# Kernel optimization log

Measured on AMD Instinct MI355X. Metric: run time of the kernel, lower is better.

Reference implementation:

```python
import jax, jax.numpy as jnp
import numpy as np

H = 24; W = 24; N = H * W            # board tokens
R = 4; BINS = (2 * R + 1) ** 2 + 1    # 82 rel-pos bins (far bin = 81)
G = 2                                  # num_global_tokens
T = N + 1 + G                          # cls + globals + board tokens = 579
D = 256; NH = 8; HD = D // NH
DEPTH = 6; MLP = int(D * 2.0)
B = 16; CIN = 10


def _ln(x, g, b):
    m = jnp.mean(x, axis=-1, keepdims=True)
    v = jnp.mean(jnp.square(x - m), axis=-1, keepdims=True)
    return (x - m) * jax.lax.rsqrt(v + 1e-5) * g + b


def _head(x, g, b, w1, b1, w2, b2):
    h = _ln(x, g, b)
    h = jax.nn.gelu(h @ w1 + b1, approximate=False)
    return h @ w2 + b2


def _forward(obs, input_w, input_b, cls_token, global_tokens, row_embed, col_embed,
             ln1_g, ln1_b, qkv_w, qkv_b, proj_w, proj_b, rel_bias,
             ln2_g, ln2_b, fc1_w, fc1_b, fc2_w, fc2_b,
             norm_g, norm_b,
             pol_ln_g, pol_ln_b, pol_w1, pol_b1, pol_w2, pol_b2,
             val_ln_g, val_ln_b, val_w1, val_b1, val_w2, val_b2,
             rel_idx):
    Bsz = obs.shape[0]
    # _tokens_from_obs: (B, C, H, W) -> (B, N, C); channel order is already [revealed, counts]
    tokens = obs.reshape(Bsz, CIN, N).transpose(0, 2, 1)
    x = tokens @ input_w + input_b                                    # (B, N, D)
    pos = (row_embed[:, None, :] + col_embed[None, :, :]).reshape(N, D)
    x = x + pos
    x = jnp.concatenate([jnp.broadcast_to(cls_token, (Bsz, 1, D)),
                         jnp.broadcast_to(global_tokens, (Bsz, G, D)),
                         x], axis=1)                                   # (B, T, D)
    scale = 1.0 / jnp.sqrt(jnp.float32(HD))

    def block(x, p):
        l1g, l1b, qw, qb, pw, pb, rb, l2g, l2b, f1w, f1b, f2w, f2b = p
        h = _ln(x, l1g, l1b)
        qkv = (h @ qw + qb).reshape(Bsz, T, 3, NH, HD)
        q, k, v = qkv[:, :, 0], qkv[:, :, 1], qkv[:, :, 2]             # (B, T, NH, HD)
        bias = rb[:, rel_idx]                                          # (NH, T, T) gathered bias
        scores = jnp.einsum('bqhd,bkhd->bhqk', q, k) * scale + bias[None]
        probs = jax.nn.softmax(scores, axis=-1)
        o = jnp.einsum('bhqk,bkhd->bqhd', probs, v).reshape(Bsz, T, D)
        x = x + o @ pw + pb
        h2 = _ln(x, l2g, l2b)
        x = x + jax.nn.gelu(h2 @ f1w + f1b, approximate=False) @ f2w + f2b
        return x, None

    params = (ln1_g, ln1_b, qkv_w, qkv_b, proj_w, proj_b, rel_bias,
              ln2_g, ln2_b, fc1_w, fc1_b, fc2_w, fc2_b)
    x, _ = jax.lax.scan(block, x, params)
    x = _ln(x, norm_g, norm_b)
    cls_tok = x[:, 0]
    token_states = x[:, 1:N + 1]   # faithful to source slice (includes the global tokens)
    logits = _head(token_states, pol_ln_g, pol_ln_b, pol_w1, pol_b1, pol_w2, pol_b2)[..., 0]  # (B, N)
    value = _head(cls_tok, val_ln_g, val_ln_b, val_w1, val_b1, val_w2, val_b2)                 # (B, 1)
    return jnp.concatenate([logits, value], axis=1)  # (B, N+1)


def setup_inputs() -> dict:
    keys = iter(jax.random.split(jax.random.key(0), 40))
    def p(shape, s=0.02):
        return jax.random.normal(next(keys), shape, jnp.float32) * s
    # _build_rel_pos_index, embedded into full (T, T) buffer with far_bin elsewhere
    coords = np.stack(np.meshgrid(np.arange(H), np.arange(W), indexing='ij'), -1).reshape(-1, 2)
    rel = coords[:, None, :] - coords[None, :, :]
    far = (np.abs(rel) > R).any(-1)
    rel = np.clip(rel, -R, R) + R
    idx = rel[..., 0] * (2 * R + 1) + rel[..., 1]
    idx = np.where(far, BINS - 1, idx)
    full = np.full((T, T), BINS - 1, np.int32)
    full[1:N + 1, 1:N + 1] = idx
    return {
        'obs': jax.random.normal(next(keys), (B, CIN, H, W), jnp.float32),
        'input_w': p((CIN, D)), 'input_b': jnp.zeros((D,)),
        'cls_token': jnp.zeros((1, 1, D)),
        'global_tokens': jnp.zeros((1, G, D)),
        'row_embed': p((H, D)), 'col_embed': p((W, D)),
        'ln1_g': jnp.ones((DEPTH, D)), 'ln1_b': jnp.zeros((DEPTH, D)),
        'qkv_w': p((DEPTH, D, 3 * D)), 'qkv_b': jnp.zeros((DEPTH, 3 * D)),
        'proj_w': p((DEPTH, D, D)), 'proj_b': jnp.zeros((DEPTH, D)),
        'rel_bias': p((DEPTH, NH, BINS)),
        'ln2_g': jnp.ones((DEPTH, D)), 'ln2_b': jnp.zeros((DEPTH, D)),
        'fc1_w': p((DEPTH, D, MLP)), 'fc1_b': jnp.zeros((DEPTH, MLP)),
        'fc2_w': p((DEPTH, MLP, D)), 'fc2_b': jnp.zeros((DEPTH, D)),
        'norm_g': jnp.ones((D,)), 'norm_b': jnp.zeros((D,)),
        'pol_ln_g': jnp.ones((D,)), 'pol_ln_b': jnp.zeros((D,)),
        'pol_w1': p((D, D)), 'pol_b1': jnp.zeros((D,)),
        'pol_w2': p((D, 1)), 'pol_b2': jnp.zeros((1,)),
        'val_ln_g': jnp.ones((D,)), 'val_ln_b': jnp.zeros((D,)),
        'val_w1': p((D, D)), 'val_b1': jnp.zeros((D,)),
        'val_w2': p((D, 1)), 'val_b2': jnp.zeros((1,)),
        'rel_idx': jnp.asarray(full),
    }


def reference(obs, input_w, input_b, cls_token, global_tokens, row_embed, col_embed,
              ln1_g, ln1_b, qkv_w, qkv_b, proj_w, proj_b, rel_bias,
              ln2_g, ln2_b, fc1_w, fc1_b, fc2_w, fc2_b,
              norm_g, norm_b,
              pol_ln_g, pol_ln_b, pol_w1, pol_b1, pol_w2, pol_b2,
              val_ln_g, val_ln_b, val_w1, val_b1, val_w2, val_b2,
              rel_idx):
    return _forward(obs, input_w, input_b, cls_token, global_tokens, row_embed, col_embed,
                    ln1_g, ln1_b, qkv_w, qkv_b, proj_w, proj_b, rel_bias,
                    ln2_g, ln2_b, fc1_w, fc1_b, fc2_w, fc2_b,
                    norm_g, norm_b,
                    pol_ln_g, pol_ln_b, pol_w1, pol_b1, pol_w2, pol_b2,
                    val_ln_g, val_ln_b, val_w1, val_b1, val_w2, val_b2,
                    rel_idx)
```

## Files before the change

### kernel.cpp

```cpp
#include <hip/hip_runtime.h>
#include <math.h>

constexpr int Hc = 24, Wc = 24, Nc = 576, BINSc = 82, Gc = 2;
constexpr int Tc = Nc + 1 + Gc;
constexpr int Dc = 256, NHc = 8, HDc = 32, DEPTHc = 6, MLPc = 512;
constexpr int Bc = 16, CINc = 10;
constexpr int BT = Bc * Tc;
constexpr float SCALE = 0.17677669529663687f;

typedef _Float16 f16;
typedef _Float16 f16x8 __attribute__((ext_vector_type(8)));
typedef _Float16 f16x16 __attribute__((ext_vector_type(16)));
typedef float f32x4 __attribute__((ext_vector_type(4)));

constexpr size_t QK_ST   = (size_t)BT * 256;
constexpr int    VT_PAD  = 640;
constexpr size_t VT_ST   = (size_t)Bc * NHc * 32 * VT_PAD;
constexpr size_t OFF_KH  = 2 * QK_ST;
constexpr size_t OFF_VTH = 4 * QK_ST;
constexpr size_t OFF_BIAS = 4 * QK_ST + 2 * VT_ST;
constexpr int    BPAD    = 580;
constexpr size_t R_F16   = OFF_BIAS + (size_t)NHc * Tc * BPAD;
constexpr size_t R_FLOATS = 8707904;

__device__ __forceinline__ int xcd_swz(int d, int nwg) {
    const int q = nwg >> 3, r = nwg & 7;
    const int x = d & 7, s = d >> 3;
    return x * q + (x < r ? x : r) + s;
}

__device__ __forceinline__ float gelu_f(float x) {
    return 0.5f * x * (1.0f + erff(x * 0.70710678118654752f));
}

__device__ __forceinline__ float block_sum256(float v, float* s4) {
    #pragma unroll
    for (int off = 32; off > 0; off >>= 1) v += __shfl_down(v, off, 64);
    __syncthreads();
    if ((threadIdx.x & 63) == 0) s4[threadIdx.x >> 6] = v;
    __syncthreads();
    return s4[0] + s4[1] + s4[2] + s4[3];
}

__global__ __launch_bounds__(256) void embed_kernel(
        const float* __restrict__ obs, const float* __restrict__ iw,
        const float* __restrict__ ib, const float* __restrict__ cls,
        const float* __restrict__ glob, const float* __restrict__ rowe,
        const float* __restrict__ cole, float* __restrict__ x) {
    int t = blockIdx.x, b = blockIdx.y, d = threadIdx.x;
    float v;
    if (t == 0) {
        v = cls[d];
    } else if (t <= Gc) {
        v = glob[(t - 1) * Dc + d];
    } else {
        int n = t - 1 - Gc;
        float acc = ib[d];
        #pragma unroll
        for (int c = 0; c < CINc; ++c)
            acc = fmaf(obs[(b * CINc + c) * Nc + n], iw[c * Dc + d], acc);
        v = acc + rowe[(n / Wc) * Dc + d] + cole[(n % Wc) * Dc + d];
    }
    x[((size_t)b * Tc + t) * Dc + d] = v;
}

__global__ __launch_bounds__(256) void ln4_kernel(
        const float* __restrict__ x, const float* __restrict__ g,
        const float* __restrict__ b, float* __restrict__ out, int nrows) {
    const int w = threadIdx.x >> 6, l = threadIdx.x & 63;
    const int row = blockIdx.x * 4 + w;
    if (row >= nrows) return;
    const float4 v = *reinterpret_cast<const float4*>(x + (size_t)row * Dc + l * 4);
    float s = v.x + v.y + v.z + v.w;
    #pragma unroll
    for (int mk = 1; mk < 64; mk <<= 1) s += __shfl_xor(s, mk, 64);
    const float m = s * (1.0f / 256.0f);
    const float4 d = make_float4(v.x - m, v.y - m, v.z - m, v.w - m);
    float vs = d.x * d.x + d.y * d.y + d.z * d.z + d.w * d.w;
    #pragma unroll
    for (int mk = 1; mk < 64; mk <<= 1) vs += __shfl_xor(vs, mk, 64);
    const float rs = rsqrtf(vs * (1.0f / 256.0f) + 1e-5f);
    const float4 gg = *reinterpret_cast<const float4*>(g + l * 4);
    const float4 bb = *reinterpret_cast<const float4*>(b + l * 4);
    *reinterpret_cast<float4*>(out + (size_t)row * Dc + l * 4) =
        make_float4(d.x * rs * gg.x + bb.x, d.y * rs * gg.y + bb.y,
                    d.z * rs * gg.z + bb.z, d.w * rs * gg.w + bb.w);
}

__global__ __launch_bounds__(256) void lnsel4_kernel(
        const float* __restrict__ xn, const float* __restrict__ g,
        const float* __restrict__ b, float* __restrict__ out) {
    const int w = threadIdx.x >> 6, l = threadIdx.x & 63;
    const int rr = blockIdx.x * 4 + w;
    const int bb = rr / Nc, n = rr % Nc;
    const float* xr = xn + ((size_t)bb * Tc + 1 + n) * Dc;
    const float4 v = *reinterpret_cast<const float4*>(xr + l * 4);
    float s = v.x + v.y + v.z + v.w;
    #pragma unroll
    for (int mk = 1; mk < 64; mk <<= 1) s += __shfl_xor(s, mk, 64);
    const float m = s * (1.0f / 256.0f);
    const float4 d = make_float4(v.x - m, v.y - m, v.z - m, v.w - m);
    float vs = d.x * d.x + d.y * d.y + d.z * d.z + d.w * d.w;
    #pragma unroll
    for (int mk = 1; mk < 64; mk <<= 1) vs += __shfl_xor(vs, mk, 64);
    const float rs = rsqrtf(vs * (1.0f / 256.0f) + 1e-5f);
    const float4 gg = *reinterpret_cast<const float4*>(g + l * 4);
    const float4 bb4 = *reinterpret_cast<const float4*>(b + l * 4);
    *reinterpret_cast<float4*>(out + ((size_t)bb * Nc + n) * Dc + l * 4) =
        make_float4(d.x * rs * gg.x + bb4.x, d.y * rs * gg.y + bb4.y,
                    d.z * rs * gg.z + bb4.z, d.w * rs * gg.w + bb4.w);
}

__global__ __launch_bounds__(256) void split_w_kernel(
        const float* __restrict__ qkv_w, const float* __restrict__ proj_w,
        const float* __restrict__ fc1_w, const float* __restrict__ fc2_w,
        const float* __restrict__ pol_w1, f16* __restrict__ out) {
    int r = blockIdx.x * 256 + threadIdx.x;
    float v; f16* dst; int NK;
    if (r < 1179648) {
        int layer = r / 196608, e = r % 196608;
        int n = e >> 8, k = e & 255;
        v = qkv_w[(size_t)layer * 196608 + k * 768 + n];
        dst = out + (size_t)layer * 393216 + n * 256 + k; NK = 196608;
    } else if (r < 1572864) {
        int rr = r - 1179648; int layer = rr / 65536, e = rr % 65536;
        int n = e >> 8, k = e & 255;
        v = proj_w[(size_t)layer * 65536 + k * 256 + n];
        dst = out + 2359296 + (size_t)layer * 131072 + n * 256 + k; NK = 65536;
    } else if (r < 2359296) {
        int rr = r - 1572864; int layer = rr / 131072, e = rr % 131072;
        int n = e >> 8, k = e & 255;
        v = fc1_w[(size_t)layer * 131072 + k * 512 + n];
        dst = out + 3145728 + (size_t)layer * 262144 + n * 256 + k; NK = 131072;
    } else if (r < 3145728) {
        int rr = r - 2359296; int layer = rr / 131072, e = rr % 131072;
        int n = e >> 9, k = e & 511;
        v = fc2_w[(size_t)layer * 131072 + k * 256 + n];
        dst = out + 4718592 + (size_t)layer * 262144 + n * 512 + k; NK = 131072;
    } else if (r < 3211264) {
        int rr = r - 3145728; int n = rr >> 8, k = rr & 255;
        v = pol_w1[k * 256 + n];
        dst = out + 6291456 + n * 256 + k; NK = 65536;
    } else return;
    f16 h = (f16)v;
    dst[0] = h;
    dst[NK] = (f16)(v - (float)h);
}

__global__ __launch_bounds__(256) void biasgen_kernel(
        const float* __restrict__ relb, const int* __restrict__ relidx,
        f16* __restrict__ bias) {
    const int q = blockIdx.x, h = blockIdx.y;
    const size_t rowo = ((size_t)h * Tc + q) * BPAD;
    const int* ridx = relidx + q * Tc;
    const float* rb = relb + h * BINSc;
    for (int kp = threadIdx.x; kp * 2 + 1 < Tc; kp += 256) {
        f16 b0 = (f16)rb[ridx[kp * 2]];
        f16 b1 = (f16)rb[ridx[kp * 2 + 1]];
        unsigned pk = (unsigned)__builtin_bit_cast(unsigned short, b0) |
                      ((unsigned)__builtin_bit_cast(unsigned short, b1) << 16);
        *reinterpret_cast<unsigned*>(&bias[rowo + kp * 2]) = pk;
    }
    if (threadIdx.x == 0)
        bias[rowo + Tc - 1] = (f16)rb[ridx[Tc - 1]];
}

__device__ __forceinline__ int swz(int r, int g) {
    return r * 40 + ((g ^ ((r >> 3) & 3)) << 3);
}
template <int ACT, bool RES>
__global__ __launch_bounds__(256) void mgemm_kernel(
        const float* __restrict__ A, const f16* __restrict__ WT,
        const float* __restrict__ bias, const float* __restrict__ res,
        float* __restrict__ C, int M, int N, int K, int nbx) {
    constexpr int BM = 128, BN = 64, BK = 32;
    __shared__ f16 Ah[BM * 40], Al[BM * 40];
    __shared__ f16 Bh[BN * 40], Bl[BN * 40];
    const int tid = threadIdx.x;
    const int v = xcd_swz(blockIdx.x, gridDim.x);
    const int m0 = (v / nbx) * BM, n0 = (v % nbx) * BN;
    const int w = tid >> 6, l = tid & 63;
    const int wm = (w >> 1) * 64, wn = (w & 1) * 32;
    const int lg = l >> 4, lr = l & 15;
    f32x4 acc[4][2] = {};
    const int sa_row = tid >> 1, sa_kc = (tid & 1) * 16;
    const int sb_part = tid >> 7;
    const int sb_n = (tid & 127) >> 1, sb_kc = (tid & 1) * 16;

    for (int k0 = 0; k0 < K; k0 += BK) {
        {
            int gr = m0 + sa_row; if (gr >= M) gr = M - 1;
            const float4* src = reinterpret_cast<const float4*>(
                A + (size_t)gr * K + k0 + sa_kc);
            f16x8 hv0, hv1, lv0, lv1;
            #pragma unroll
            for (int c = 0; c < 4; ++c) {
                float4 v4 = src[c];
                f16 h0 = (f16)v4.x, h1 = (f16)v4.y, h2 = (f16)v4.z, h3 = (f16)v4.w;
                f16 l0 = (f16)(v4.x - (float)h0), l1 = (f16)(v4.y - (float)h1);
                f16 l2 = (f16)(v4.z - (float)h2), l3 = (f16)(v4.w - (float)h3);
                if (c < 2) {
                    hv0[c * 4 + 0] = h0; hv0[c * 4 + 1] = h1;
                    hv0[c * 4 + 2] = h2; hv0[c * 4 + 3] = h3;
                    lv0[c * 4 + 0] = l0; lv0[c * 4 + 1] = l1;
                    lv0[c * 4 + 2] = l2; lv0[c * 4 + 3] = l3;
                } else {
                    hv1[(c - 2) * 4 + 0] = h0; hv1[(c - 2) * 4 + 1] = h1;
                    hv1[(c - 2) * 4 + 2] = h2; hv1[(c - 2) * 4 + 3] = h3;
                    lv1[(c - 2) * 4 + 0] = l0; lv1[(c - 2) * 4 + 1] = l1;
                    lv1[(c - 2) * 4 + 2] = l2; lv1[(c - 2) * 4 + 3] = l3;
                }
            }
            const int g0 = sa_kc >> 3;
            *reinterpret_cast<f16x8*>(&Ah[swz(sa_row, g0)])     = hv0;
            *reinterpret_cast<f16x8*>(&Ah[swz(sa_row, g0 + 1)]) = hv1;
            *reinterpret_cast<f16x8*>(&Al[swz(sa_row, g0)])     = lv0;
            *reinterpret_cast<f16x8*>(&Al[swz(sa_row, g0 + 1)]) = lv1;
        }
        {
            const f16x8* src = reinterpret_cast<const f16x8*>(
                WT + (size_t)sb_part * N * K + (size_t)(n0 + sb_n) * K + k0 + sb_kc);
            f16* dbase = sb_part ? Bl : Bh;
            const int g0 = sb_kc >> 3;
            *reinterpret_cast<f16x8*>(&dbase[swz(sb_n, g0)])     = src[0];
            *reinterpret_cast<f16x8*>(&dbase[swz(sb_n, g0 + 1)]) = src[1];
        }
        __syncthreads();
        f16x8 afh[4], afl[4], bfh[2], bfl[2];
        #pragma unroll
        for (int mi = 0; mi < 4; ++mi) {
            int row = wm + mi * 16 + lr;
            afh[mi] = *reinterpret_cast<const f16x8*>(&Ah[swz(row, lg)]);
            afl[mi] = *reinterpret_cast<const f16x8*>(&Al[swz(row, lg)]);
        }
        #pragma unroll
        for (int ni = 0; ni < 2; ++ni) {
            int col = wn + ni * 16 + lr;
            bfh[ni] = *reinterpret_cast<const f16x8*>(&Bh[swz(col, lg)]);
            bfl[ni] = *reinterpret_cast<const f16x8*>(&Bl[swz(col, lg)]);
        }
        #pragma unroll
        for (int mi = 0; mi < 4; ++mi)
            #pragma unroll
            for (int ni = 0; ni < 2; ++ni) {
                acc[mi][ni] = __builtin_amdgcn_mfma_f32_16x16x32_f16(
                    afh[mi], bfh[ni], acc[mi][ni], 0, 0, 0);
                acc[mi][ni] = __builtin_amdgcn_mfma_f32_16x16x32_f16(
                    afh[mi], bfl[ni], acc[mi][ni], 0, 0, 0);
                acc[mi][ni] = __builtin_amdgcn_mfma_f32_16x16x32_f16(
                    afl[mi], bfh[ni], acc[mi][ni], 0, 0, 0);
            }
        __syncthreads();
    }
    float bv[2];
    #pragma unroll
    for (int ni = 0; ni < 2; ++ni) bv[ni] = bias[n0 + wn + ni * 16 + lr];
    #pragma unroll
    for (int mi = 0; mi < 4; ++mi) {
        #pragma unroll
        for (int r = 0; r < 4; ++r) {
            int grow = m0 + wm + mi * 16 + lg * 4 + r;
            if (grow >= M) continue;
            if constexpr (ACT == 2) {
                f16* base = (f16*)C;
                const int bb = grow / Tc;
                const int tt = grow - bb * Tc;
                #pragma unroll
                for (int ni = 0; ni < 2; ++ni) {
                    const int gcol = n0 + wn + ni * 16 + lr;
                    float vv = acc[mi][ni][r] + bv[ni];
                    if (gcol < 256) {
                        vv *= SCALE;
                        f16 hh = (f16)vv;
                        base[(size_t)grow * 256 + gcol] = hh;
                        base[QK_ST + (size_t)grow * 256 + gcol] = (f16)(vv - (float)hh);
                    } else if (gcol < 512) {
                        f16 hh = (f16)vv;
                        base[OFF_KH + (size_t)grow * 256 + (gcol - 256)] = hh;
                        base[OFF_KH + QK_ST + (size_t)grow * 256 + (gcol - 256)] =
                            (f16)(vv - (float)hh);
                    } else {
                        const int e = gcol - 512;
                        const int hh_ = e >> 5, dd = e & 31;
                        const size_t o =
                            ((size_t)((bb * NHc + hh_) * 32 + dd)) * VT_PAD + tt;
                        f16 hh = (f16)vv;
                        base[OFF_VTH + o] = hh;
                        base[OFF_VTH + VT_ST + o] = (f16)(vv - (float)hh);
                    }
                }
            } else {
                #pragma unroll
                for (int ni = 0; ni < 2; ++ni) {
                    int gcol = n0 + wn + ni * 16 + lr;
                    float vv = acc[mi][ni][r] + bv[ni];
                    if (ACT == 1) vv = gelu_f(vv);
                    if (RES) vv += res[(size_t)grow * N + gcol];
                    C[(size_t)grow * N + gcol] = vv;
                }
            }
        }
    }
}

__global__ __launch_bounds__(256, 4) void mattn2_kernel(
        const f16* __restrict__ qsp, float* __restrict__ o) {
    __shared__ __align__(16) f16 Kh_s[64][40], Kl_s[64][40];
    __shared__ __align__(16) f16 VTh_s[32][72], VTl_s[32][72];
    __shared__ __align__(16) f16 Ph_s[4][16][72], Pl_s[4][16][72];
    const f16* __restrict__ Kh_g  = qsp + OFF_KH;
    const f16* __restrict__ VTh_g = qsp + OFF_VTH;
    const f16* __restrict__ bias_g = qsp + OFF_BIAS;

    const int tid = threadIdx.x;
    const int v = xcd_swz(blockIdx.x, 1280);
    const int bh = v / 10, qt = v - bh * 10;
    const int b = bh >> 3, h = bh & 7;
    const int q0 = qt * 64;
    const int w = tid >> 6, l = tid & 63;
    const int lr = l & 15, lg = l >> 4;

    int qrow = q0 + w * 16 + lr; if (qrow >= Tc) qrow = Tc - 1;
    const f16* qp = qsp + ((size_t)(b * Tc + qrow)) * 256 + h * 32 + lg * 8;
    const f16x8 Qh = *reinterpret_cast<const f16x8*>(qp);
    const f16x8 Ql = *reinterpret_cast<const f16x8*>(qp + QK_ST);
    const int myq = q0 + w * 16 + lg * 4;

    int boff[4];
    #pragma unroll
    for (int r = 0; r < 4; ++r) {
        int qq = myq + r; if (qq >= Tc) qq = Tc - 1;
        boff[r] = (h * Tc + qq) * BPAD;
    }

    const int skrow = tid >> 2, skc = (tid & 3) * 8;
    const int svd = tid >> 3, svc = (tid & 7) * 8;
    const f16* vrow = VTh_g + ((size_t)((b * NHc + h) * 32 + svd)) * VT_PAD;

    struct KV { f16x8 kh, kl, vh, vl; };
    auto load_kv = [&](int k0) {
        KV r;
        int gk = k0 + skrow; if (gk >= Tc) gk = Tc - 1;
        const f16* kp = Kh_g + ((size_t)(b * Tc + gk)) * 256 + h * 32 + skc;
        r.kh = *reinterpret_cast<const f16x8*>(kp);
        r.kl = *reinterpret_cast<const f16x8*>(kp + QK_ST);
        const f16* vp = vrow + k0 + svc;
        r.vh = *reinterpret_cast<const f16x8*>(vp);
        r.vl = *reinterpret_cast<const f16x8*>(vp + VT_ST);
        return r;
    };
    auto load_bias = [&](int k0) {
        f16x16 bv;
        #pragma unroll
        for (int r = 0; r < 4; ++r)
            #pragma unroll
            for (int j = 0; j < 4; ++j) {
                int kk = k0 + j * 16 + lr; if (kk >= Tc) kk = Tc - 1;
                bv[r * 4 + j] = bias_g[boff[r] + kk];
            }
        return bv;
    };

    KV pA = load_kv(0);
    KV pB = load_kv(64);
    f16x16 bias_c = load_bias(0), bias_n;

    float m_run[4], l_run[4];
    f32x4 Oacc[2] = {};
    #pragma unroll
    for (int r = 0; r < 4; ++r) { m_run[r] = -1e30f; l_run[r] = 0.f; }

    for (int t = 0; t < 10; ++t) {
        const int k0 = t * 64;
        __syncthreads();
        *reinterpret_cast<f16x8*>(&Kh_s[skrow][skc]) = pA.kh;
        *reinterpret_cast<f16x8*>(&Kl_s[skrow][skc]) = pA.kl;
        *reinterpret_cast<f16x8*>(&VTh_s[svd][svc]) = pA.vh;
        *reinterpret_cast<f16x8*>(&VTl_s[svd][svc]) = pA.vl;
        pA = pB;
        if (t + 2 < 10) pB = load_kv(k0 + 128);
        __syncthreads();
        if (t + 1 < 10) bias_n = load_bias(k0 + 64);
        f32x4 sc[4];
        #pragma unroll
        for (int j = 0; j < 4; ++j) {
            const f16x8 kh = *reinterpret_cast<const f16x8*>(&Kh_s[j * 16 + lr][lg * 8]);
            const f16x8 kl = *reinterpret_cast<const f16x8*>(&Kl_s[j * 16 + lr][lg * 8]);
            f32x4 s = {};
            s = __builtin_amdgcn_mfma_f32_16x16x32_f16(Qh, kh, s, 0, 0, 0);
            s = __builtin_amdgcn_mfma_f32_16x16x32_f16(Qh, kl, s, 0, 0, 0);
            s = __builtin_amdgcn_mfma_f32_16x16x32_f16(Ql, kh, s, 0, 0, 0);
            sc[j] = s;
        }
        #pragma unroll
        for (int r = 0; r < 4; ++r)
            #pragma unroll
            for (int j = 0; j < 4; ++j) {
                const int kk = k0 + j * 16 + lr;
                float vv = sc[j][r] + (float)bias_c[r * 4 + j];
                sc[j][r] = (kk < Tc) ? vv : -1e30f;
            }
        #pragma unroll
        for (int r = 0; r < 4; ++r) {
            float tm = fmaxf(fmaxf(sc[0][r], sc[1][r]), fmaxf(sc[2][r], sc[3][r]));
            #pragma unroll
            for (int mk = 1; mk < 16; mk <<= 1) tm = fmaxf(tm, __shfl_xor(tm, mk, 64));
            const float mn = fmaxf(m_run[r], tm);
            const float resc = __expf(m_run[r] - mn);
            m_run[r] = mn;
            float ls = 0.f;
            #pragma unroll
            for (int j = 0; j < 4; ++j) {
                sc[j][r] = __expf(sc[j][r] - mn);
                ls += sc[j][r];
            }
            #pragma unroll
            for (int mk = 1; mk < 16; mk <<= 1) ls += __shfl_xor(ls, mk, 64);
            l_run[r] = l_run[r] * resc + ls;
            Oacc[0][r] *= resc; Oacc[1][r] *= resc;
            const int prow = lg * 4 + r;
            #pragma unroll
            for (int j = 0; j < 4; ++j) {
                const float p = sc[j][r];
                const f16 ph = (f16)p;
                Ph_s[w][prow][j * 16 + lr] = ph;
                Pl_s[w][prow][j * 16 + lr] = (f16)(p - (float)ph);
            }
        }
        #pragma unroll
        for (int kc = 0; kc < 2; ++kc) {
            const f16x8 Pa = *reinterpret_cast<const f16x8*>(&Ph_s[w][lr][kc * 32 + lg * 8]);
            const f16x8 Pb = *reinterpret_cast<const f16x8*>(&Pl_s[w][lr][kc * 32 + lg * 8]);
            #pragma unroll
            for (int dt = 0; dt < 2; ++dt) {
                const f16x8 vh = *reinterpret_cast<const f16x8*>(&VTh_s[dt * 16 + lr][kc * 32 + lg * 8]);
                const f16x8 vl = *reinterpret_cast<const f16x8*>(&VTl_s[dt * 16 + lr][kc * 32 + lg * 8]);
                Oacc[dt] = __builtin_amdgcn_mfma_f32_16x16x32_f16(Pa, vh, Oacc[dt], 0, 0, 0);
                Oacc[dt] = __builtin_amdgcn_mfma_f32_16x16x32_f16(Pa, vl, Oacc[dt], 0, 0, 0);
                Oacc[dt] = __builtin_amdgcn_mfma_f32_16x16x32_f16(Pb, vh, Oacc[dt], 0, 0, 0);
            }
        }
        if (t + 1 < 10) bias_c = bias_n;
    }
    #pragma unroll
    for (int r = 0; r < 4; ++r) {
        const int qq = myq + r;
        if (qq < Tc) {
            const float inv = 1.0f / l_run[r];
            float* op = o + ((size_t)b * Tc + qq) * Dc + h * HDc;
            op[lr]      = Oacc[0][r] * inv;
            op[16 + lr] = Oacc[1][r] * inv;
        }
    }
}

__global__ __launch_bounds__(256) void logits_kernel(
        const float* __restrict__ ph, const float* __restrict__ w2,
        const float* __restrict__ b2, float* __restrict__ out) {
    __shared__ float s4[4];
    size_t r = blockIdx.x;
    int bb = (int)(r / Nc), n = (int)(r % Nc);
    float v = ph[r * Dc + threadIdx.x] * w2[threadIdx.x];
    float s = block_sum256(v, s4);
    if (threadIdx.x == 0) out[bb * (Nc + 1) + n] = s + b2[0];
}

__global__ __launch_bounds__(256) void value_kernel(
        const float* __restrict__ xn, const float* __restrict__ g,
        const float* __restrict__ b, const float* __restrict__ w1,
        const float* __restrict__ b1, const float* __restrict__ w2,
        const float* __restrict__ b2, float* __restrict__ out) {
    __shared__ float s4[4];
    __shared__ float ts[Dc];
    const int bb = blockIdx.x, tid = threadIdx.x;
    float v = xn[(size_t)bb * Tc * Dc + tid];
    float m = block_sum256(v, s4) * (1.0f / 256.0f);
    float d = v - m;
    float var = block_sum256(d * d, s4) * (1.0f / 256.0f);
    ts[tid] = d * rsqrtf(var + 1e-5f) * g[tid] + b[tid];
    __syncthreads();
    float acc = b1[tid];
    #pragma unroll 8
    for (int i = 0; i < Dc; ++i) acc = fmaf(ts[i], w1[i * Dc + tid], acc);
    float hv = gelu_f(acc) * w2[tid];
    float s = block_sum256(hv, s4);
    if (tid == 0) out[bb * (Nc + 1) + Nc] = s + b2[0];
}

extern "C" void kernel_launch(void* const* d_in, const int* in_sizes, int n_in,
                              void* d_out, int out_size, void* d_ws, size_t ws_size,
                              hipStream_t stream) {
    const float* obs      = (const float*)d_in[0];
    const float* input_w  = (const float*)d_in[1];
    const float* input_b  = (const float*)d_in[2];
    const float* cls_tok  = (const float*)d_in[3];
    const float* glob_tok = (const float*)d_in[4];
    const float* row_emb  = (const float*)d_in[5];
    const float* col_emb  = (const float*)d_in[6];
    const float* ln1_g    = (const float*)d_in[7];
    const float* ln1_b    = (const float*)d_in[8];
    const float* qkv_w    = (const float*)d_in[9];
    const float* qkv_b    = (const float*)d_in[10];
    const float* proj_w   = (const float*)d_in[11];
    const float* proj_b   = (const float*)d_in[12];
    const float* rel_bias = (const float*)d_in[13];
    const float* ln2_g    = (const float*)d_in[14];
    const float* ln2_b    = (const float*)d_in[15];
    const float* fc1_w    = (const float*)d_in[16];
    const float* fc1_b    = (const float*)d_in[17];
    const float* fc2_w    = (const float*)d_in[18];
    const float* fc2_b    = (const float*)d_in[19];
    const float* norm_g   = (const float*)d_in[20];
    const float* norm_b   = (const float*)d_in[21];
    const float* pol_ln_g = (const float*)d_in[22];
    const float* pol_ln_b = (const float*)d_in[23];
    const float* pol_w1   = (const float*)d_in[24];
    const float* pol_b1   = (const float*)d_in[25];
    const float* pol_w2   = (const float*)d_in[26];
    const float* pol_b2   = (const float*)d_in[27];
    const float* val_ln_g = (const float*)d_in[28];
    const float* val_ln_b = (const float*)d_in[29];
    const float* val_w1   = (const float*)d_in[30];
    const float* val_b1   = (const float*)d_in[31];
    const float* val_w2   = (const float*)d_in[32];
    const float* val_b2   = (const float*)d_in[33];
    const int*   rel_idx  = (const int*)d_in[34];
    float* out = (float*)d_out;

    float* ws = (float*)d_ws;
    const size_t SZ_XD = (size_t)BT * Dc;
    float* X  = ws;
    float* Hb = ws + SZ_XD;
    float* R  = ws + 2 * SZ_XD;
    f16* qsp = (f16*)R;
    f16* bias_g = qsp + OFF_BIAS;
    float* MLPH = R;
    float* PT = R;
    float* PH = R + (size_t)Bc * Nc * Dc;
    f16* wsplit = (f16*)(R + R_FLOATS);

    auto qkvT = [&](int l) { return wsplit + (size_t)l * 393216; };
    auto projT = [&](int l) { return wsplit + 2359296 + (size_t)l * 131072; };
    auto fc1T = [&](int l) { return wsplit + 3145728 + (size_t)l * 262144; };
    auto fc2T = [&](int l) { return wsplit + 4718592 + (size_t)l * 262144; };
    f16* polT = wsplit + 6291456;

    split_w_kernel<<<12544, 256, 0, stream>>>(
        qkv_w, proj_w, fc1_w, fc2_w, pol_w1, wsplit);

    embed_kernel<<<dim3(Tc, Bc), 256, 0, stream>>>(
        obs, input_w, input_b, cls_tok, glob_tok, row_emb, col_emb, X);

    for (int l = 0; l < DEPTHc; ++l) {
        ln4_kernel<<<(BT + 3) / 4, 256, 0, stream>>>(
            X, ln1_g + l * Dc, ln1_b + l * Dc, Hb, BT);
        mgemm_kernel<2, false><<<876, 256, 0, stream>>>(
            Hb, qkvT(l), qkv_b + l * 3 * Dc, nullptr, (float*)qsp, BT, 3 * Dc, Dc, 12);
        biasgen_kernel<<<dim3(Tc, NHc), 256, 0, stream>>>(
            rel_bias + l * NHc * BINSc, rel_idx, bias_g);
        mattn2_kernel<<<1280, 256, 0, stream>>>(qsp, Hb);
        mgemm_kernel<0, true><<<292, 256, 0, stream>>>(
            Hb, projT(l), proj_b + l * Dc, X, X, BT, Dc, Dc, 4);
        ln4_kernel<<<(BT + 3) / 4, 256, 0, stream>>>(
            X, ln2_g + l * Dc, ln2_b + l * Dc, Hb, BT);
        mgemm_kernel<1, false><<<584, 256, 0, stream>>>(
            Hb, fc1T(l), fc1_b + l * MLPc, nullptr, MLPH, BT, MLPc, Dc, 8);
        mgemm_kernel<0, true><<<292, 256, 0, stream>>>(
            MLPH, fc2T(l), fc2_b + l * Dc, X, X, BT, Dc, MLPc, 4);
    }

    ln4_kernel<<<(BT + 3) / 4, 256, 0, stream>>>(X, norm_g, norm_b, Hb, BT);
    lnsel4_kernel<<<Bc * Nc / 4, 256, 0, stream>>>(Hb, pol_ln_g, pol_ln_b, PT);
    mgemm_kernel<1, false><<<288, 256, 0, stream>>>(
        PT, polT, pol_b1, nullptr, PH, Bc * Nc, Dc, Dc, 4);
    logits_kernel<<<Bc * Nc, 256, 0, stream>>>(PH, pol_w2, pol_b2, out);
    value_kernel<<<Bc, 256, 0, stream>>>(
        Hb, val_ln_g, val_ln_b, val_w1, val_b1, val_w2, val_b2, out);
}
```

Measured before the change: 1.314 ms.

## Fuse LayerNorm apply into GEMM A-load and compute softmax denominator via MFMA

```diff
diff --git a/kernel.cpp b/kernel.cpp
--- a/kernel.cpp
+++ b/kernel.cpp
@@ -62,6 +62,24 @@
         v = acc + rowe[(n / Wc) * Dc + d] + cole[(n % Wc) * Dc + d];
     }
     x[((size_t)b * Tc + t) * Dc + d] = v;
+}
+
+__global__ __launch_bounds__(256) void lnstats_kernel(
+        const float* __restrict__ x, float2* __restrict__ st, int nrows) {
+    const int w = threadIdx.x >> 6, l = threadIdx.x & 63;
+    const int row = blockIdx.x * 4 + w;
+    if (row >= nrows) return;
+    const float4 v = *reinterpret_cast<const float4*>(x + (size_t)row * Dc + l * 4);
+    float s = v.x + v.y + v.z + v.w;
+    #pragma unroll
+    for (int mk = 1; mk < 64; mk <<= 1) s += __shfl_xor(s, mk, 64);
+    const float m = s * (1.0f / 256.0f);
+    float vs = (v.x - m) * (v.x - m) + (v.y - m) * (v.y - m) +
+               (v.z - m) * (v.z - m) + (v.w - m) * (v.w - m);
+    #pragma unroll
+    for (int mk = 1; mk < 64; mk <<= 1) vs += __shfl_xor(vs, mk, 64);
+    if (l == 0)
+        st[row] = make_float2(m, rsqrtf(vs * (1.0f / 256.0f) + 1e-5f));
 }
 
 __global__ __launch_bounds__(256) void ln4_kernel(
@@ -168,11 +186,13 @@
 __device__ __forceinline__ int swz(int r, int g) {
     return r * 40 + ((g ^ ((r >> 3) & 3)) << 3);
 }
-template <int ACT, bool RES>
+template <int ACT, bool RES, bool LNA>
 __global__ __launch_bounds__(256) void mgemm_kernel(
         const float* __restrict__ A, const f16* __restrict__ WT,
         const float* __restrict__ bias, const float* __restrict__ res,
-        float* __restrict__ C, int M, int N, int K, int nbx) {
+        float* __restrict__ C, int M, int N, int K, int nbx,
+        const float2* __restrict__ lnst, const float* __restrict__ lng,
+        const float* __restrict__ lnb) {
     constexpr int BM = 128, BN = 64, BK = 32;
     __shared__ f16 Ah[BM * 40], Al[BM * 40];
     __shared__ f16 Bh[BN * 40], Bl[BN * 40];
@@ -187,15 +207,28 @@
     const int sb_part = tid >> 7;
     const int sb_n = (tid & 127) >> 1, sb_kc = (tid & 1) * 16;
 
+    int gr = m0 + sa_row; if (gr >= M) gr = M - 1;
+    float mu = 0.f, rsd = 1.f;
+    if constexpr (LNA) { float2 s2 = lnst[gr]; mu = s2.x; rsd = s2.y; }
+
     for (int k0 = 0; k0 < K; k0 += BK) {
         {
-            int gr = m0 + sa_row; if (gr >= M) gr = M - 1;
             const float4* src = reinterpret_cast<const float4*>(
                 A + (size_t)gr * K + k0 + sa_kc);
             f16x8 hv0, hv1, lv0, lv1;
             #pragma unroll
             for (int c = 0; c < 4; ++c) {
                 float4 v4 = src[c];
+                if constexpr (LNA) {
+                    const float4 g4 = *reinterpret_cast<const float4*>(
+                        lng + k0 + sa_kc + c * 4);
+                    const float4 b4 = *reinterpret_cast<const float4*>(
+                        lnb + k0 + sa_kc + c * 4);
+                    v4.x = (v4.x - mu) * rsd * g4.x + b4.x;
+                    v4.y = (v4.y - mu) * rsd * g4.y + b4.y;
+                    v4.z = (v4.z - mu) * rsd * g4.z + b4.z;
+                    v4.w = (v4.w - mu) * rsd * g4.w + b4.w;
+                }
                 f16 h0 = (f16)v4.x, h1 = (f16)v4.y, h2 = (f16)v4.z, h3 = (f16)v4.w;
                 f16 l0 = (f16)(v4.x - (float)h0), l1 = (f16)(v4.y - (float)h1);
                 f16 l2 = (f16)(v4.z - (float)h2), l3 = (f16)(v4.w - (float)h3);
@@ -314,8 +347,9 @@
 
     const int tid = threadIdx.x;
     const int v = xcd_swz(blockIdx.x, 1280);
-    const int bh = v / 10, qt = v - bh * 10;
-    const int b = bh >> 3, h = bh & 7;
+    const int h = v / 160;
+    const int rem = v - h * 160;
+    const int b = rem / 10, qt = rem - b * 10;
     const int q0 = qt * 64;
     const int w = tid >> 6, l = tid & 63;
     const int lr = l & 15, lg = l >> 4;
@@ -365,10 +399,15 @@
     KV pB = load_kv(64);
     f16x16 bias_c = load_bias(0), bias_n;
 
-    float m_run[4], l_run[4];
+    f16x8 kOnes;
+    #pragma unroll
+    for (int e = 0; e < 8; ++e) kOnes[e] = (f16)1.0f;
+
+    float m_run[4];
     f32x4 Oacc[2] = {};
-    #pragma unroll
-    for (int r = 0; r < 4; ++r) { m_run[r] = -1e30f; l_run[r] = 0.f; }
+    f32x4 Oext = {};
+    #pragma unroll
+    for (int r = 0; r < 4; ++r) m_run[r] = -1e30f;
 
     for (int t = 0; t < 10; ++t) {
         const int k0 = t * 64;
@@ -386,20 +425,18 @@
         for (int j = 0; j < 4; ++j) {
             const f16x8 kh = *reinterpret_cast<const f16x8*>(&Kh_s[j * 16 + lr][lg * 8]);
             const f16x8 kl = *reinterpret_cast<const f16x8*>(&Kl_s[j * 16 + lr][lg * 8]);
-            f32x4 s = {};
+            f32x4 s = {(float)bias_c[j], (float)bias_c[4 + j],
+                       (float)bias_c[8 + j], (float)bias_c[12 + j]};
             s = __builtin_amdgcn_mfma_f32_16x16x32_f16(Qh, kh, s, 0, 0, 0);
             s = __builtin_amdgcn_mfma_f32_16x16x32_f16(Qh, kl, s, 0, 0, 0);
             s = __builtin_amdgcn_mfma_f32_16x16x32_f16(Ql, kh, s, 0, 0, 0);
             sc[j] = s;
         }
         #pragma unroll
-        for (int r = 0; r < 4; ++r)
-            #pragma unroll
-            for (int j = 0; j < 4; ++j) {
-                const int kk = k0 + j * 16 + lr;
-                float vv = sc[j][r] + (float)bias_c[r * 4 + j];
-                sc[j][r] = (kk < Tc) ? vv : -1e30f;
-            }
+        for (int j = 0; j < 4; ++j) {
+            const int kk = k0 + j * 16 + lr;
+            if (kk >= Tc) { sc[j][0] = sc[j][1] = sc[j][2] = sc[j][3] = -1e30f; }
+        }
         #pragma unroll
         for (int r = 0; r < 4; ++r) {
             float tm = fmaxf(fmaxf(sc[0][r], sc[1][r]), fmaxf(sc[2][r], sc[3][r]));
@@ -408,20 +445,11 @@
             const float mn = fmaxf(m_run[r], tm);
             const float resc = __expf(m_run[r] - mn);
             m_run[r] = mn;
-            float ls = 0.f;
-            #pragma unroll
-            for (int j = 0; j < 4; ++j) {
-                sc[j][r] = __expf(sc[j][r] - mn);
-                ls += sc[j][r];
-            }
-            #pragma unroll
-            for (int mk = 1; mk < 16; mk <<= 1) ls += __shfl_xor(ls, mk, 64);
-            l_run[r] = l_run[r] * resc + ls;
-            Oacc[0][r] *= resc; Oacc[1][r] *= resc;
+            Oacc[0][r] *= resc; Oacc[1][r] *= resc; Oext[r] *= resc;
             const int prow = lg * 4 + r;
             #pragma unroll
             for (int j = 0; j < 4; ++j) {
-                const float p = sc[j][r];
+                const float p = __expf(sc[j][r] - mn);
                 const f16 ph = (f16)p;
                 Ph_s[w][prow][j * 16 + lr] = ph;
                 Pl_s[w][prow][j * 16 + lr] = (f16)(p - (float)ph);
@@ -439,6 +467,8 @@
                 Oacc[dt] = __builtin_amdgcn_mfma_f32_16x16x32_f16(Pa, vl, Oacc[dt], 0, 0, 0);
                 Oacc[dt] = __builtin_amdgcn_mfma_f32_16x16x32_f16(Pb, vh, Oacc[dt], 0, 0, 0);
             }
+            Oext = __builtin_amdgcn_mfma_f32_16x16x32_f16(Pa, kOnes, Oext, 0, 0, 0);
+            Oext = __builtin_amdgcn_mfma_f32_16x16x32_f16(Pb, kOnes, Oext, 0, 0, 0);
         }
         if (t + 1 < 10) bias_c = bias_n;
     }
@@ -446,7 +476,7 @@
     for (int r = 0; r < 4; ++r) {
         const int qq = myq + r;
         if (qq < Tc) {
-            const float inv = 1.0f / l_run[r];
+            const float inv = 1.0f / Oext[r];
             float* op = o + ((size_t)b * Tc + qq) * Dc + h * HDc;
             op[lr]      = Oacc[0][r] * inv;
             op[16 + lr] = Oacc[1][r] * inv;
@@ -538,6 +568,7 @@
     float* PT = R;
     float* PH = R + (size_t)Bc * Nc * Dc;
     f16* wsplit = (f16*)(R + R_FLOATS);
+    float2* lnst = (float2*)(wsplit + 6422528);
 
     auto qkvT = [&](int l) { return wsplit + (size_t)l * 393216; };
     auto projT = [&](int l) { return wsplit + 2359296 + (size_t)l * 131072; };
@@ -552,27 +583,30 @@
         obs, input_w, input_b, cls_tok, glob_tok, row_emb, col_emb, X);
 
     for (int l = 0; l < DEPTHc; ++l) {
-        ln4_kernel<<<(BT + 3) / 4, 256, 0, stream>>>(
-            X, ln1_g + l * Dc, ln1_b + l * Dc, Hb, BT);
-        mgemm_kernel<2, false><<<876, 256, 0, stream>>>(
-            Hb, qkvT(l), qkv_b + l * 3 * Dc, nullptr, (float*)qsp, BT, 3 * Dc, Dc, 12);
+        lnstats_kernel<<<(BT + 3) / 4, 256, 0, stream>>>(X, lnst, BT);
+        mgemm_kernel<2, false, true><<<876, 256, 0, stream>>>(
+            X, qkvT(l), qkv_b + l * 3 * Dc, nullptr, (float*)qsp, BT, 3 * Dc, Dc, 12,
+            lnst, ln1_g + l * Dc, ln1_b + l * Dc);
         biasgen_kernel<<<dim3(Tc, NHc), 256, 0, stream>>>(
             rel_bias + l * NHc * BINSc, rel_idx, bias_g);
         mattn2_kernel<<<1280, 256, 0, stream>>>(qsp, Hb);
-        mgemm_kernel<0, true><<<292, 256, 0, stream>>>(
-            Hb, projT(l), proj_b + l * Dc, X, X, BT, Dc, Dc, 4);
-        ln4_kernel<<<(BT + 3) / 4, 256, 0, stream>>>(
-            X, ln2_g + l * Dc, ln2_b + l * Dc, Hb, BT);
-        mgemm_kernel<1, false><<<584, 256, 0, stream>>>(
-            Hb, fc1T(l), fc1_b + l * MLPc, nullptr, MLPH, BT, MLPc, Dc, 8);
-        mgemm_kernel<0, true><<<292, 256, 0, stream>>>(
-            MLPH, fc2T(l), fc2_b + l * Dc, X, X, BT, Dc, MLPc, 4);
+        mgemm_kernel<0, true, false><<<292, 256, 0, stream>>>(
+            Hb, projT(l), proj_b + l * Dc, X, X, BT, Dc, Dc, 4,
+            nullptr, nullptr, nullptr);
+        lnstats_kernel<<<(BT + 3) / 4, 256, 0, stream>>>(X, lnst, BT);
+        mgemm_kernel<1, false, true><<<584, 256, 0, stream>>>(
+            X, fc1T(l), fc1_b + l * MLPc, nullptr, MLPH, BT, MLPc, Dc, 8,
+            lnst, ln2_g + l * Dc, ln2_b + l * Dc);
+        mgemm_kernel<0, true, false><<<292, 256, 0, stream>>>(
+            MLPH, fc2T(l), fc2_b + l * Dc, X, X, BT, Dc, MLPc, 4,
+            nullptr, nullptr, nullptr);
     }
 
     ln4_kernel<<<(BT + 3) / 4, 256, 0, stream>>>(X, norm_g, norm_b, Hb, BT);
     lnsel4_kernel<<<Bc * Nc / 4, 256, 0, stream>>>(Hb, pol_ln_g, pol_ln_b, PT);
-    mgemm_kernel<1, false><<<288, 256, 0, stream>>>(
-        PT, polT, pol_b1, nullptr, PH, Bc * Nc, Dc, Dc, 4);
+    mgemm_kernel<1, false, false><<<288, 256, 0, stream>>>(
+        PT, polT, pol_b1, nullptr, PH, Bc * Nc, Dc, Dc, 4,
+        nullptr, nullptr, nullptr);
     logits_kernel<<<Bc * Nc, 256, 0, stream>>>(PH, pol_w2, pol_b2, out);
     value_kernel<<<Bc, 256, 0, stream>>>(
         Hb, val_ln_g, val_ln_b, val_w1, val_b1, val_w2, val_b2, out);
```

Result: no change. 1.300 ms (-1.1%).
